# Kernel tuning notes

Measured on AMD Instinct MI355X. Metric: run time of the kernel, lower is better.

The kernel has to match this reference:

```python
import jax, jax.numpy as jnp
import numpy as np

N_NODES = 50000
N_EDGES = 800000
IN_DIM = 512
OUT_DIM = 512


def setup_inputs() -> dict:
    key = jax.random.key(0)
    ks = jax.random.split(key, 8)
    x = jax.random.normal(ks[0], (N_NODES, IN_DIM), dtype=jnp.float32)
    edge_index = jax.random.randint(ks[1], (2, N_EDGES), 0, N_NODES, dtype=jnp.int64)
    s = 1.0 / np.sqrt(IN_DIM)
    # SAGEConv params: lin_l (applied to aggregated neighbors, with bias),
    # lin_r (applied to root/self features, no bias). Two convs: loc and scale.
    Wl1 = jax.random.uniform(ks[2], (OUT_DIM, IN_DIM), jnp.float32, -s, s)
    bl1 = jnp.zeros((OUT_DIM,), jnp.float32)
    Wr1 = jax.random.uniform(ks[3], (OUT_DIM, IN_DIM), jnp.float32, -s, s)
    Wl2 = jax.random.uniform(ks[4], (OUT_DIM, IN_DIM), jnp.float32, -s, s)
    bl2 = jnp.zeros((OUT_DIM,), jnp.float32)
    Wr2 = jax.random.uniform(ks[5], (OUT_DIM, IN_DIM), jnp.float32, -s, s)
    return {"x": x, "edge_index": edge_index,
            "Wl1": Wl1, "bl1": bl1, "Wr1": Wr1,
            "Wl2": Wl2, "bl2": bl2, "Wr2": Wr2}


def _sage_conv(x, agg, Wl, bl, Wr):
    # lin_l(sum-aggregated neighbors) + lin_r(x)
    return agg @ Wl.T + bl + x @ Wr.T


def reference(x, edge_index, Wl1, bl1, Wr1, Wl2, bl2, Wr2):
    src, dst = edge_index[0], edge_index[1]
    # sum aggregation of source features into destination nodes: [N, in_dim]
    agg = jax.ops.segment_sum(x[src], dst, num_segments=N_NODES)
    loc = _sage_conv(x, agg, Wl1, bl1, Wr1)
    loc = jnp.clip(loc, -100.0, 100.0)
    scale = jax.nn.softplus(_sage_conv(x, agg, Wl2, bl2, Wr2)) + 0.001
    scale = jnp.minimum(scale, 100.0)
    return (loc, scale)
```

## Files before the change

kernel.cpp:

```cpp
#include <hip/hip_runtime.h>
#include <stdint.h>

#define N_NODES 50000
#define N_EDGES 800000
#define IN_DIM 512
#define OUT_DIM 512
#define KDIM 1024
#define NDIM 1024

typedef __bf16 bf16x8 __attribute__((ext_vector_type(8)));
typedef float f32x4 __attribute__((ext_vector_type(4)));

__device__ __forceinline__ unsigned short f2bf(float f) {
    union { float f; unsigned u; } c; c.f = f;
    unsigned u = c.u;
    u += 0x7fffu + ((u >> 16) & 1u);
    return (unsigned short)(u >> 16);
}
__device__ __forceinline__ float bf2f(unsigned short h) {
    union { unsigned u; float f; } c; c.u = ((unsigned)h) << 16;
    return c.f;
}

__global__ void xconv_kernel(const float* __restrict__ x, unsigned short* __restrict__ xb) {
    int i = blockIdx.x * blockDim.x + threadIdx.x;
    const int n4 = N_NODES * IN_DIM / 4;
    if (i < n4) {
        float4 v = ((const float4*)x)[i];
        ushort4 o;
        o.x = f2bf(v.x); o.y = f2bf(v.y); o.z = f2bf(v.z); o.w = f2bf(v.w);
        ((ushort4*)xb)[i] = o;
    }
}

__global__ void count_kernel(const int* __restrict__ ei, int* __restrict__ counts) {
    int i = blockIdx.x * blockDim.x + threadIdx.x;
    if (i < N_EDGES) {
        int dst = ei[N_EDGES + i];
        dst = min(max(dst, 0), N_NODES - 1);
        atomicAdd(&counts[dst], 1);
    }
}

__global__ void scan_kernel(const int* __restrict__ cnt, int* __restrict__ offs,
                            int* __restrict__ cursor, int n) {
    __shared__ int warp_sums[16];
    __shared__ int s_base;
    int tid = threadIdx.x;
    int lane = tid & 63;
    int w = tid >> 6;
    if (tid == 0) s_base = 0;
    __syncthreads();
    for (int start = 0; start < n; start += 1024) {
        int i = start + tid;
        int v = (i < n) ? cnt[i] : 0;
        int s = v;
        #pragma unroll
        for (int d = 1; d < 64; d <<= 1) {
            int t = __shfl_up(s, d, 64);
            if (lane >= d) s += t;
        }
        if (lane == 63) warp_sums[w] = s;
        __syncthreads();
        if (w == 0) {
            int ws = (lane < 16) ? warp_sums[lane] : 0;
            #pragma unroll
            for (int d = 1; d < 16; d <<= 1) {
                int t = __shfl_up(ws, d, 64);
                if (lane >= d) ws += t;
            }
            if (lane < 16) warp_sums[lane] = ws;
        }
        __syncthreads();
        int base = s_base + (w > 0 ? warp_sums[w - 1] : 0);
        int excl = base + s - v;
        if (i < n) { offs[i] = excl; cursor[i] = excl; }
        if (i == n - 1) offs[n] = excl + v;
        __syncthreads();
        if (tid == 0) s_base += warp_sums[15];
        __syncthreads();
    }
}

__global__ void fill_kernel(const int* __restrict__ ei, int* __restrict__ cursor,
                            int* __restrict__ bucket) {
    int i = blockIdx.x * blockDim.x + threadIdx.x;
    if (i < N_EDGES) {
        int src = ei[i];
        int dst = ei[N_EDGES + i];
        src = min(max(src, 0), N_NODES - 1);
        dst = min(max(dst, 0), N_NODES - 1);
        int pos = atomicAdd(&cursor[dst], 1);
        bucket[pos] = src;
    }
}

__global__ __launch_bounds__(256) void aggregate_kernel(
    const unsigned short* __restrict__ xb, const int* __restrict__ offs,
    const int* __restrict__ bucket, unsigned short* __restrict__ aggb) {
    int n = blockIdx.x;
    int t = threadIdx.x;
    int beg = offs[n], end = offs[n + 1];
    const unsigned* xw = (const unsigned*)xb;
    float ax0 = 0.f, ay0 = 0.f, ax1 = 0.f, ay1 = 0.f;
    float ax2 = 0.f, ay2 = 0.f, ax3 = 0.f, ay3 = 0.f;
    int e = beg;
    for (; e + 4 <= end; e += 4) {
        int s0 = bucket[e + 0];
        int s1 = bucket[e + 1];
        int s2 = bucket[e + 2];
        int s3 = bucket[e + 3];
        unsigned v0 = xw[(size_t)s0 * (IN_DIM / 2) + t];
        unsigned v1 = xw[(size_t)s1 * (IN_DIM / 2) + t];
        unsigned v2 = xw[(size_t)s2 * (IN_DIM / 2) + t];
        unsigned v3 = xw[(size_t)s3 * (IN_DIM / 2) + t];
        ax0 += bf2f((unsigned short)(v0 & 0xffffu)); ay0 += bf2f((unsigned short)(v0 >> 16));
        ax1 += bf2f((unsigned short)(v1 & 0xffffu)); ay1 += bf2f((unsigned short)(v1 >> 16));
        ax2 += bf2f((unsigned short)(v2 & 0xffffu)); ay2 += bf2f((unsigned short)(v2 >> 16));
        ax3 += bf2f((unsigned short)(v3 & 0xffffu)); ay3 += bf2f((unsigned short)(v3 >> 16));
    }
    for (; e < end; ++e) {
        int s = bucket[e];
        unsigned v = xw[(size_t)s * (IN_DIM / 2) + t];
        ax0 += bf2f((unsigned short)(v & 0xffffu));
        ay0 += bf2f((unsigned short)(v >> 16));
    }
    float ax = (ax0 + ax1) + (ax2 + ax3);
    float ay = (ay0 + ay1) + (ay2 + ay3);
    unsigned o = (unsigned)f2bf(ax) | ((unsigned)f2bf(ay) << 16);
    ((unsigned*)aggb)[(size_t)n * (IN_DIM / 2) + t] = o;
}

__global__ void wconv_kernel(const float* __restrict__ Wl1, const float* __restrict__ Wr1,
                             const float* __restrict__ Wl2, const float* __restrict__ Wr2,
                             unsigned short* __restrict__ Wb) {
    int i = blockIdx.x * blockDim.x + threadIdx.x;
    if (i < NDIM * KDIM) {
        int n = i >> 10, k = i & 1023;
        const float* src;
        if (n < 512) src = (k < 512) ? Wl1 : Wr1;
        else         src = (k < 512) ? Wl2 : Wr2;
        int nn = n & 511, kk = k & 511;
        Wb[i] = f2bf(src[nn * 512 + kk]);
    }
}

#define BM 128
#define BN 128
#define BK 64

__device__ __forceinline__ void async_copy16(const void* g, void* lds) {
    __builtin_amdgcn_global_load_lds((const __attribute__((address_space(1))) void*)g,
                                     (__attribute__((address_space(3))) void*)lds, 16, 0, 0);
}

__global__ __launch_bounds__(256, 2) void gemm_kernel(
    const unsigned short* __restrict__ aggb,
    const unsigned short* __restrict__ xb,
    const unsigned short* __restrict__ Wb,
    const float* __restrict__ bl1, const float* __restrict__ bl2,
    float* __restrict__ out) {
    constexpr int M = N_NODES;
    __shared__ unsigned short sA[BM * BK];
    __shared__ unsigned short sB[BN * BK];

    int n0 = blockIdx.x * BN;
    int m0 = blockIdx.y * BM;
    int tid = threadIdx.x;
    int lane = tid & 63;
    int w = tid >> 6;
    int wm = (w >> 1) * 64, wn = (w & 1) * 64;

    f32x4 acc[4][4] = {};

    int fr = lane & 15, q = lane >> 4;
    int sl0 = ((q ^ (fr & 7)) << 3);
    int sl1 = (((q + 4) ^ (fr & 7)) << 3);

    for (int k0 = 0; k0 < KDIM; k0 += BK) {
        const unsigned short* Asrc;
        int ak;
        if (k0 < 512) { Asrc = aggb; ak = k0; } else { Asrc = xb; ak = k0 - 512; }
        #pragma unroll
        for (int iss = 0; iss < 4; ++iss) {
            int C = iss * 256 + tid;
            int r = C >> 3, p = C & 7;
            int gr = m0 + r; if (gr >= M) gr = M - 1;
            const unsigned short* g = Asrc + (size_t)gr * 512 + ak + ((p ^ (r & 7)) << 3);
            async_copy16(g, sA + (size_t)(iss * 256 + w * 64) * 8);
        }
        #pragma unroll
        for (int iss = 0; iss < 4; ++iss) {
            int C = iss * 256 + tid;
            int r = C >> 3, p = C & 7;
            const unsigned short* g = Wb + (size_t)(n0 + r) * KDIM + k0 + ((p ^ (r & 7)) << 3);
            async_copy16(g, sB + (size_t)(iss * 256 + w * 64) * 8);
        }
        __syncthreads();

        #pragma unroll
        for (int ksub = 0; ksub < 2; ++ksub) {
            int sl = ksub ? sl1 : sl0;
            bf16x8 af[4], bfg[4];
            #pragma unroll
            for (int i = 0; i < 4; ++i)
                af[i] = *(const bf16x8*)(sA + (wm + i * 16 + fr) * BK + sl);
            #pragma unroll
            for (int j = 0; j < 4; ++j)
                bfg[j] = *(const bf16x8*)(sB + (wn + j * 16 + fr) * BK + sl);
            #pragma unroll
            for (int i = 0; i < 4; ++i)
                #pragma unroll
                for (int j = 0; j < 4; ++j)
                    acc[i][j] = __builtin_amdgcn_mfma_f32_16x16x32_bf16(af[i], bfg[j], acc[i][j], 0, 0, 0);
        }
        __syncthreads();
    }

    bool is_scale = (n0 >= 512);
    const float* bias = is_scale ? bl2 : bl1;
    float* obase = out + (is_scale ? (size_t)N_NODES * OUT_DIM : 0);
    int ncol0 = is_scale ? (n0 - 512) : n0;
    int rq = lane >> 4;
    #pragma unroll
    for (int i = 0; i < 4; ++i) {
        #pragma unroll
        for (int j = 0; j < 4; ++j) {
            int colg = ncol0 + wn + j * 16 + fr;
            float b = bias[colg];
            #pragma unroll
            for (int r = 0; r < 4; ++r) {
                int rowg = m0 + wm + i * 16 + rq * 4 + r;
                if (rowg < M) {
                    float v = acc[i][j][r] + b;
                    float res;
                    if (is_scale) {
                        float sp = fmaxf(v, 0.f) + __logf(1.f + __expf(-fabsf(v)));
                        res = fminf(sp + 0.001f, 100.f);
                    } else {
                        res = fminf(fmaxf(v, -100.f), 100.f);
                    }
                    __builtin_nontemporal_store(res, &obase[(size_t)rowg * OUT_DIM + colg]);
                }
            }
        }
    }
}

extern "C" void kernel_launch(void* const* d_in, const int* in_sizes, int n_in,
                              void* d_out, int out_size, void* d_ws, size_t ws_size,
                              hipStream_t stream) {
    const float* x       = (const float*)d_in[0];
    const int* ei        = (const int*)d_in[1];
    const float* Wl1     = (const float*)d_in[2];
    const float* bl1     = (const float*)d_in[3];
    const float* Wr1     = (const float*)d_in[4];
    const float* Wl2     = (const float*)d_in[5];
    const float* bl2     = (const float*)d_in[6];
    const float* Wr2     = (const float*)d_in[7];
    float* out = (float*)d_out;

    char* ws = (char*)d_ws;
    size_t off = 0;
    auto alloc = [&](size_t bytes) -> void* {
        void* p = ws + off;
        off = (off + bytes + 255) & ~(size_t)255;
        return p;
    };
    unsigned short* xb    = (unsigned short*)alloc((size_t)N_NODES * IN_DIM * 2);
    unsigned short* aggb  = (unsigned short*)alloc((size_t)N_NODES * IN_DIM * 2);
    unsigned short* Wb    = (unsigned short*)alloc((size_t)NDIM * KDIM * 2);
    int* counts           = (int*)alloc((size_t)(N_NODES + 1) * 4);
    int* offs             = (int*)alloc((size_t)(N_NODES + 1) * 4);
    int* cursor           = (int*)alloc((size_t)N_NODES * 4);
    int* bucket           = (int*)alloc((size_t)N_EDGES * 4);

    hipMemsetAsync(counts, 0, (size_t)(N_NODES + 1) * 4, stream);

    xconv_kernel<<<(N_NODES * IN_DIM / 4 + 255) / 256, 256, 0, stream>>>(x, xb);
    count_kernel<<<(N_EDGES + 255) / 256, 256, 0, stream>>>(ei, counts);
    scan_kernel<<<1, 1024, 0, stream>>>(counts, offs, cursor, N_NODES);
    fill_kernel<<<(N_EDGES + 255) / 256, 256, 0, stream>>>(ei, cursor, bucket);
    aggregate_kernel<<<N_NODES, 256, 0, stream>>>(xb, offs, bucket, aggb);
    wconv_kernel<<<(NDIM * KDIM + 255) / 256, 256, 0, stream>>>(Wl1, Wr1, Wl2, Wr2, Wb);

    dim3 g(NDIM / BN, (N_NODES + BM - 1) / BM);
    gemm_kernel<<<g, 256, 0, stream>>>(aggb, xb, Wb, bl1, bl2, out);
}
```

Measured before the change: 673.9 us.

## Parallelize offset scan, unroll aggregation gathers by 8, widen GEMM tile to 256 columns

Replaces the single-block serial prefix scan with a three-kernel block-parallel scan (local scan, scan of block sums, apply). Widens the aggregation loop to eight in-flight gathers per thread to raise memory-level parallelism. Doubles the GEMM N tile to 256, so each wave holds a 64x128 accumulator tile and reuses each A fragment across more MFMAs. The larger tile doubles accumulator registers and B-tile LDS, which may reduce occupancy below the requested two blocks per CU.

```diff
diff --git a/kernel.cpp b/kernel.cpp
--- a/kernel.cpp
+++ b/kernel.cpp
@@ -42,43 +42,59 @@
     }
 }
 
-__global__ void scan_kernel(const int* __restrict__ cnt, int* __restrict__ offs,
-                            int* __restrict__ cursor, int n) {
+__global__ __launch_bounds__(1024) void scan_local_kernel(
+    const int* __restrict__ cnt, int* __restrict__ offs,
+    int* __restrict__ bsums, int n) {
     __shared__ int warp_sums[16];
-    __shared__ int s_base;
     int tid = threadIdx.x;
     int lane = tid & 63;
     int w = tid >> 6;
-    if (tid == 0) s_base = 0;
+    int i = blockIdx.x * 1024 + tid;
+    int v = (i < n) ? cnt[i] : 0;
+    int s = v;
+    #pragma unroll
+    for (int d = 1; d < 64; d <<= 1) {
+        int t = __shfl_up(s, d, 64);
+        if (lane >= d) s += t;
+    }
+    if (lane == 63) warp_sums[w] = s;
     __syncthreads();
-    for (int start = 0; start < n; start += 1024) {
-        int i = start + tid;
-        int v = (i < n) ? cnt[i] : 0;
-        int s = v;
-        #pragma unroll
-        for (int d = 1; d < 64; d <<= 1) {
-            int t = __shfl_up(s, d, 64);
-            if (lane >= d) s += t;
-        }
-        if (lane == 63) warp_sums[w] = s;
-        __syncthreads();
-        if (w == 0) {
-            int ws = (lane < 16) ? warp_sums[lane] : 0;
-            #pragma unroll
-            for (int d = 1; d < 16; d <<= 1) {
-                int t = __shfl_up(ws, d, 64);
-                if (lane >= d) ws += t;
-            }
-            if (lane < 16) warp_sums[lane] = ws;
-        }
-        __syncthreads();
-        int base = s_base + (w > 0 ? warp_sums[w - 1] : 0);
-        int excl = base + s - v;
-        if (i < n) { offs[i] = excl; cursor[i] = excl; }
-        if (i == n - 1) offs[n] = excl + v;
-        __syncthreads();
-        if (tid == 0) s_base += warp_sums[15];
-        __syncthreads();
+    if (w == 0) {
+        int ws = (lane < 16) ? warp_sums[lane] : 0;
+        #pragma unroll
+        for (int d = 1; d < 16; d <<= 1) {
+            int t = __shfl_up(ws, d, 64);
+            if (lane >= d) ws += t;
+        }
+        if (lane < 16) warp_sums[lane] = ws;
+    }
+    __syncthreads();
+    int base = (w > 0 ? warp_sums[w - 1] : 0);
+    if (i < n) offs[i] = base + s - v;
+    if (tid == 1023) bsums[blockIdx.x] = base + s;
+}
+
+__global__ void scan_bsums_kernel(int* __restrict__ bsums, int nb) {
+    int lane = threadIdx.x & 63;
+    int v = (lane < nb) ? bsums[lane] : 0;
+    int s = v;
+    #pragma unroll
+    for (int d = 1; d < 64; d <<= 1) {
+        int t = __shfl_up(s, d, 64);
+        if (lane >= d) s += t;
+    }
+    if (lane < nb) bsums[lane] = s - v;
+}
+
+__global__ __launch_bounds__(1024) void scan_apply_kernel(
+    int* __restrict__ offs, int* __restrict__ cursor,
+    const int* __restrict__ bsums, const int* __restrict__ cnt, int n) {
+    int i = blockIdx.x * 1024 + threadIdx.x;
+    if (i < n) {
+        int o = offs[i] + bsums[blockIdx.x];
+        offs[i] = o;
+        cursor[i] = o;
+        if (i == n - 1) offs[n] = o + cnt[i];
     }
 }
 
@@ -102,32 +118,30 @@
     int t = threadIdx.x;
     int beg = offs[n], end = offs[n + 1];
     const unsigned* xw = (const unsigned*)xb;
-    float ax0 = 0.f, ay0 = 0.f, ax1 = 0.f, ay1 = 0.f;
-    float ax2 = 0.f, ay2 = 0.f, ax3 = 0.f, ay3 = 0.f;
+    float ax[8] = {}, ay[8] = {};
     int e = beg;
-    for (; e + 4 <= end; e += 4) {
-        int s0 = bucket[e + 0];
-        int s1 = bucket[e + 1];
-        int s2 = bucket[e + 2];
-        int s3 = bucket[e + 3];
-        unsigned v0 = xw[(size_t)s0 * (IN_DIM / 2) + t];
-        unsigned v1 = xw[(size_t)s1 * (IN_DIM / 2) + t];
-        unsigned v2 = xw[(size_t)s2 * (IN_DIM / 2) + t];
-        unsigned v3 = xw[(size_t)s3 * (IN_DIM / 2) + t];
-        ax0 += bf2f((unsigned short)(v0 & 0xffffu)); ay0 += bf2f((unsigned short)(v0 >> 16));
-        ax1 += bf2f((unsigned short)(v1 & 0xffffu)); ay1 += bf2f((unsigned short)(v1 >> 16));
-        ax2 += bf2f((unsigned short)(v2 & 0xffffu)); ay2 += bf2f((unsigned short)(v2 >> 16));
-        ax3 += bf2f((unsigned short)(v3 & 0xffffu)); ay3 += bf2f((unsigned short)(v3 >> 16));
+    for (; e + 8 <= end; e += 8) {
+        int idx[8];
+        unsigned v[8];
+        #pragma unroll
+        for (int u = 0; u < 8; ++u) idx[u] = bucket[e + u];
+        #pragma unroll
+        for (int u = 0; u < 8; ++u) v[u] = xw[(size_t)idx[u] * (IN_DIM / 2) + t];
+        #pragma unroll
+        for (int u = 0; u < 8; ++u) {
+            ax[u] += bf2f((unsigned short)(v[u] & 0xffffu));
+            ay[u] += bf2f((unsigned short)(v[u] >> 16));
+        }
     }
     for (; e < end; ++e) {
         int s = bucket[e];
         unsigned v = xw[(size_t)s * (IN_DIM / 2) + t];
-        ax0 += bf2f((unsigned short)(v & 0xffffu));
-        ay0 += bf2f((unsigned short)(v >> 16));
-    }
-    float ax = (ax0 + ax1) + (ax2 + ax3);
-    float ay = (ay0 + ay1) + (ay2 + ay3);
-    unsigned o = (unsigned)f2bf(ax) | ((unsigned)f2bf(ay) << 16);
+        ax[0] += bf2f((unsigned short)(v & 0xffffu));
+        ay[0] += bf2f((unsigned short)(v >> 16));
+    }
+    float sx = ((ax[0] + ax[1]) + (ax[2] + ax[3])) + ((ax[4] + ax[5]) + (ax[6] + ax[7]));
+    float sy = ((ay[0] + ay[1]) + (ay[2] + ay[3])) + ((ay[4] + ay[5]) + (ay[6] + ay[7]));
+    unsigned o = (unsigned)f2bf(sx) | ((unsigned)f2bf(sy) << 16);
     ((unsigned*)aggb)[(size_t)n * (IN_DIM / 2) + t] = o;
 }
 
@@ -146,7 +160,7 @@
 }
 
 #define BM 128
-#define BN 128
+#define BN 256
 #define BK 64
 
 __device__ __forceinline__ void async_copy16(const void* g, void* lds) {
@@ -169,9 +183,9 @@
     int tid = threadIdx.x;
     int lane = tid & 63;
     int w = tid >> 6;
-    int wm = (w >> 1) * 64, wn = (w & 1) * 64;
-
-    f32x4 acc[4][4] = {};
+    int wm = (w >> 1) * 64, wn = (w & 1) * 128;
+
+    f32x4 acc[4][8] = {};
 
     int fr = lane & 15, q = lane >> 4;
     int sl0 = ((q ^ (fr & 7)) << 3);
@@ -190,7 +204,7 @@
             async_copy16(g, sA + (size_t)(iss * 256 + w * 64) * 8);
         }
         #pragma unroll
-        for (int iss = 0; iss < 4; ++iss) {
+        for (int iss = 0; iss < 8; ++iss) {
             int C = iss * 256 + tid;
             int r = C >> 3, p = C & 7;
             const unsigned short* g = Wb + (size_t)(n0 + r) * KDIM + k0 + ((p ^ (r & 7)) << 3);
@@ -201,17 +215,17 @@
         #pragma unroll
         for (int ksub = 0; ksub < 2; ++ksub) {
             int sl = ksub ? sl1 : sl0;
-            bf16x8 af[4], bfg[4];
+            bf16x8 af[4], bfg[8];
             #pragma unroll
             for (int i = 0; i < 4; ++i)
                 af[i] = *(const bf16x8*)(sA + (wm + i * 16 + fr) * BK + sl);
             #pragma unroll
-            for (int j = 0; j < 4; ++j)
+            for (int j = 0; j < 8; ++j)
                 bfg[j] = *(const bf16x8*)(sB + (wn + j * 16 + fr) * BK + sl);
             #pragma unroll
             for (int i = 0; i < 4; ++i)
                 #pragma unroll
-                for (int j = 0; j < 4; ++j)
+                for (int j = 0; j < 8; ++j)
                     acc[i][j] = __builtin_amdgcn_mfma_f32_16x16x32_bf16(af[i], bfg[j], acc[i][j], 0, 0, 0);
         }
         __syncthreads();
@@ -225,7 +239,7 @@
     #pragma unroll
     for (int i = 0; i < 4; ++i) {
         #pragma unroll
-        for (int j = 0; j < 4; ++j) {
+        for (int j = 0; j < 8; ++j) {
             int colg = ncol0 + wn + j * 16 + fr;
             float b = bias[colg];
             #pragma unroll
@@ -274,12 +288,17 @@
     int* offs             = (int*)alloc((size_t)(N_NODES + 1) * 4);
     int* cursor           = (int*)alloc((size_t)N_NODES * 4);
     int* bucket           = (int*)alloc((size_t)N_EDGES * 4);
+    int* bsums            = (int*)alloc(64 * 4);
 
     hipMemsetAsync(counts, 0, (size_t)(N_NODES + 1) * 4, stream);
+
+    const int nb = (N_NODES + 1023) / 1024;
 
     xconv_kernel<<<(N_NODES * IN_DIM / 4 + 255) / 256, 256, 0, stream>>>(x, xb);
     count_kernel<<<(N_EDGES + 255) / 256, 256, 0, stream>>>(ei, counts);
-    scan_kernel<<<1, 1024, 0, stream>>>(counts, offs, cursor, N_NODES);
+    scan_local_kernel<<<nb, 1024, 0, stream>>>(counts, offs, bsums, N_NODES);
+    scan_bsums_kernel<<<1, 64, 0, stream>>>(bsums, nb);
+    scan_apply_kernel<<<nb, 1024, 0, stream>>>(offs, cursor, bsums, counts, N_NODES);
     fill_kernel<<<(N_EDGES + 255) / 256, 256, 0, stream>>>(ei, cursor, bucket);
     aggregate_kernel<<<N_NODES, 256, 0, stream>>>(xb, offs, bucket, aggb);
     wconv_kernel<<<(NDIM * KDIM + 255) / 256, 256, 0, stream>>>(Wl1, Wr1, Wl2, Wr2, Wb);
```

New measurement: 647.8 us. -3.9%, faster.
